# Kernel optimization log

Measured on AMD Instinct MI355X. Metric: run time of the kernel, lower is better.

## Reference

```python
import jax, jax.numpy as jnp
import numpy as np

N = 100_000   # nodes
E = 1_600_000 # edges
G = 128       # graphs in batch
DIN, DOUT = 100, 200


def setup_inputs() -> dict:
    key = jax.random.key(0)
    ks = jax.random.split(key, 12)
    def lin_w(k, fan_in, fan_out):
        return (jax.random.normal(k, (fan_in, fan_out), jnp.float32) / np.sqrt(fan_in)).astype(jnp.float32)
    return {
        "x": jax.random.normal(ks[0], (N, DIN), jnp.float32),
        "edge_index": jax.random.randint(ks[1], (2, E), 0, N, dtype=jnp.int32),
        "batch": jnp.sort(jax.random.randint(ks[2], (N,), 0, G, dtype=jnp.int32)),
        "W1": lin_w(ks[3], DIN, DOUT),  "b1": jnp.zeros((DOUT,), jnp.float32),
        "Wc": lin_w(ks[4], DOUT, DOUT), "bc": jnp.zeros((DOUT,), jnp.float32),
        "W2": lin_w(ks[5], DOUT, DOUT), "b2": jnp.zeros((DOUT,), jnp.float32),
        "W3": lin_w(ks[6], DOUT, DOUT), "b3": jnp.zeros((DOUT,), jnp.float32),
        "Wcls": lin_w(ks[7], DOUT, 2),  "bcls": jnp.zeros((2,), jnp.float32),
    }


def gcn_conv(x, W, b, src, dst, n_nodes):
    """PyG GCNConv: D^{-1/2}(A+I)D^{-1/2} X W + b, symmetric norm with self-loops."""
    h = x @ W  # [N, Dout]
    # degree at targets including the self-loop (+1)
    deg = jax.ops.segment_sum(jnp.ones((src.shape[0],), x.dtype), dst, num_segments=n_nodes) + 1.0
    dinv = jax.lax.rsqrt(deg)  # [N]
    # gather -> normalize -> scatter-add (messages along edges)
    msg = h[src] * (dinv[src] * dinv[dst])[:, None]          # [E, Dout]
    agg = jax.ops.segment_sum(msg, dst, num_segments=n_nodes)  # [N, Dout]
    # self-loop contribution handled analytically: norm_ii = dinv[i]^2
    agg = agg + h * (dinv * dinv)[:, None]
    return agg + b


def reference(x, edge_index, batch, W1, b1, Wc, bc, W2, b2, W3, b3, Wcls, bcls):
    src, dst = edge_index[0], edge_index[1]
    h = jax.nn.relu(gcn_conv(x, W1, b1, src, dst, N))
    # dropout is identity at eval time
    h = h @ Wc + bc
    h = jax.nn.relu(gcn_conv(h, W2, b2, src, dst, N))
    h = gcn_conv(h, W3, b3, src, dst, N)
    pooled = jax.ops.segment_max(h, batch, num_segments=G)  # global max pool -> [G, Dout]
    logits = pooled @ Wcls + bcls
    return jax.nn.softmax(logits, axis=1)
```

## Files before the change

kernel.cpp:

```cpp
#include <hip/hip_runtime.h>
#include <stdint.h>

#define N_NODES 100000
#define N_EDGES 1600000
#define N_GRAPHS 128
#define DIN 100
#define DOUT 200
#define LDH 200
#define LDX 128

#define NB 391
#define BCAP 5120
#define EPB 2048
#define NBLK 782

typedef unsigned short u16;
typedef unsigned int u32;
typedef _Float16 f16;
typedef f16 half8 __attribute__((ext_vector_type(8)));
typedef f16 half4 __attribute__((ext_vector_type(4)));
typedef f16 half2v __attribute__((ext_vector_type(2)));
typedef float floatx4 __attribute__((ext_vector_type(4)));

__device__ __forceinline__ float h2f(u16 h) {
  f16 x; __builtin_memcpy(&x, &h, 2); return (float)x;
}
__device__ __forceinline__ u16 f2h(float f) {
  f16 x = (f16)f; u16 r; __builtin_memcpy(&r, &x, 2); return r;
}

__device__ __forceinline__ void pack_frag(const float* __restrict__ W, int K, int nfrag,
                                          u16* __restrict__ out, int idx) {
  if (idx >= nfrag) return;
  int lane = idx & 63;
  int t = idx >> 6;
  int ct = t % 13, ks = t / 13;
  int n = ct * 16 + (lane & 15);
  int kbase = ks * 32 + (lane >> 4) * 8;
  u16 v[8];
  #pragma unroll
  for (int j = 0; j < 8; ++j) {
    int k = kbase + j;
    float f = (k < K && n < DOUT) ? W[(size_t)k * DOUT + n] : 0.f;
    v[j] = f2h(f);
  }
  uint4 o;
  o.x = (u32)v[0] | ((u32)v[1] << 16);
  o.y = (u32)v[2] | ((u32)v[3] << 16);
  o.z = (u32)v[4] | ((u32)v[5] << 16);
  o.w = (u32)v[6] | ((u32)v[7] << 16);
  *(uint4*)(out + (size_t)idx * 8) = o;
}

#define B_GB    391
#define B_COMB  549
#define B_PK1   562
#define B_PK3   585
#define B_TOT   (585 + NBLK)
__global__ void k_prep(const int* __restrict__ batch, int* __restrict__ gstart,
                       int* __restrict__ gend, const int* __restrict__ dst,
                       int* __restrict__ histAll,
                       const float* __restrict__ Wc, const float* __restrict__ bc,
                       const float* __restrict__ W2, float* __restrict__ Wc2,
                       float* __restrict__ bc2, const float* __restrict__ W1,
                       const float* __restrict__ W3, u16* __restrict__ Wpk1,
                       u16* __restrict__ Wpk3) {
  int b = blockIdx.x, t = threadIdx.x;
  if (b < B_GB) {
    int i = b * 256 + t;
    if (i >= N_NODES) return;
    int g = batch[i];
    if (i == 0 || batch[i - 1] != g) gstart[g] = i;
    if (i == N_NODES - 1 || batch[i + 1] != g) gend[g] = i;
  } else if (b < B_COMB) {
    int gid = (b - B_GB) * 256 + t;
    if (gid >= 201 * DOUT) return;
    int r = gid / DOUT, c = gid % DOUT;
    const float* a = (r < DOUT) ? (Wc + (size_t)r * DOUT) : bc;
    float s = 0.f;
    for (int k = 0; k < DOUT; ++k) s += a[k] * W2[(size_t)k * DOUT + c];
    if (r < DOUT) Wc2[(size_t)r * DOUT + c] = s;
    else bc2[c] = s;
  } else if (b < B_PK1) {
    pack_frag(W1, DIN, 4 * 13 * 64, Wpk1, (b - B_COMB) * 256 + t);
  } else if (b < B_PK3) {
    pack_frag(W3, DOUT, 7 * 13 * 64, Wpk3, (b - B_PK1) * 256 + t);
  } else {
    __shared__ int hist[NB];
    int hb = b - B_PK3;
    int e0 = hb * EPB;
    int e1 = min(e0 + EPB, N_EDGES);
    for (int j = t; j < NB; j += 256) hist[j] = 0;
    __syncthreads();
    for (int i = e0 + t; i < e1; i += 256)
      atomicAdd(&hist[dst[i] >> 8], 1);
    __syncthreads();
    for (int j = t; j < NB; j += 256)
      histAll[(size_t)hb * NB + j] = hist[j];
  }
}

__global__ void k_scan(const int* __restrict__ histAll, int* __restrict__ baseAll,
                       int* __restrict__ gcur) {
  __shared__ int s[256];
  int j = blockIdx.x, t = threadIdx.x;
  int run = 0;
  for (int c = 0; c < NBLK; c += 256) {
    int idx = c + t;
    int v = (idx < NBLK) ? histAll[(size_t)idx * NB + j] : 0;
    s[t] = v;
    __syncthreads();
    for (int o = 1; o < 256; o <<= 1) {
      int x = (t >= o) ? s[t - o] : 0;
      __syncthreads();
      s[t] += x;
      __syncthreads();
    }
    if (idx < NBLK) baseAll[(size_t)idx * NB + j] = run + s[t] - v;
    run += s[255];
    __syncthreads();
  }
  if (t == 0) gcur[j] = run;
}

__global__ void k_scatter(const int* __restrict__ src, const int* __restrict__ dst,
                          const int* __restrict__ baseAll, uint2* __restrict__ ebuf) {
  __shared__ int cur[NB];
  int b = blockIdx.x, t = threadIdx.x;
  int e0 = b * EPB;
  int e1 = min(e0 + EPB, N_EDGES);
  for (int j = t; j < NB; j += 256) cur[j] = baseAll[(size_t)b * NB + j];
  __syncthreads();
  for (int i = e0 + t; i < e1; i += 256) {
    int d = dst[i];
    int bk = d >> 8;
    int pos = atomicAdd(&cur[bk], 1);
    if (pos < BCAP)
      ebuf[(size_t)bk * BCAP + pos] = make_uint2((u32)d, (u32)src[i]);
  }
}

__global__ void k_csr(const uint2* __restrict__ ebuf, const int* __restrict__ gcur,
                      int* __restrict__ rowptr, float* __restrict__ dinv,
                      int* __restrict__ colv) {
  __shared__ int s_cnt[256];
  __shared__ int s_cur[256];
  __shared__ int s_scan[256];
  __shared__ int s_g[NB];
  __shared__ int s_red[256];
  int b = blockIdx.x, t = threadIdx.x;
  for (int j = t; j < NB; j += 256) s_g[j] = gcur[j];
  s_cnt[t] = 0;
  __syncthreads();
  int pacc = 0;
  for (int i = t; i < b; i += 256) pacc += s_g[i];
  s_red[t] = pacc;
  __syncthreads();
  for (int o = 128; o > 0; o >>= 1) {
    if (t < o) s_red[t] += s_red[t + o];
    __syncthreads();
  }
  int base = s_red[0];
  if (b == NB - 1 && t == 0) rowptr[N_NODES] = base + s_g[b];
  int cnt = s_g[b];
  int node0 = b << 8;
  const uint2* eb = ebuf + (size_t)b * BCAP;
  for (int i = t; i < cnt; i += 256)
    atomicAdd(&s_cnt[eb[i].x & 255], 1);
  __syncthreads();
  int v = s_cnt[t];
  s_scan[t] = v;
  __syncthreads();
  for (int o = 1; o < 256; o <<= 1) {
    int x = (t >= o) ? s_scan[t - o] : 0;
    __syncthreads();
    s_scan[t] += x;
    __syncthreads();
  }
  int run = s_scan[t] - v;
  s_cur[t] = base + run;
  int node = node0 + t;
  if (node < N_NODES) {
    rowptr[node] = base + run;
    dinv[node] = rsqrtf((float)v + 1.0f);
  }
  __syncthreads();
  for (int i = t; i < cnt; i += 256) {
    uint2 e = eb[i];
    int pos = atomicAdd(&s_cur[e.x & 255], 1);
    colv[pos] = (int)e.y;
  }
}

#define P_XS  25000
#define P_TOT 25023
__global__ void k_post(const float* __restrict__ x, const float* __restrict__ dinv,
                       u16* __restrict__ xs, const float* __restrict__ Wc2,
                       u16* __restrict__ Wpk2) {
  int b = blockIdx.x, t = threadIdx.x;
  if (b < P_XS) {
    int gid = b * 256 + t;
    int node = gid >> 6, lane = gid & 63;
    if (node >= N_NODES || lane >= 50) return;
    float d = dinv[node];
    float2 vv = *(const float2*)(x + (size_t)node * DIN + lane * 2);
    half2v o; o[0] = (f16)(d * vv.x); o[1] = (f16)(d * vv.y);
    *(half2v*)(xs + (size_t)node * LDX + lane * 2) = o;
  } else {
    pack_frag(Wc2, DOUT, 7 * 13 * 64, Wpk2, (b - P_XS) * 256 + t);
  }
}

template <int NKS>
__global__ __launch_bounds__(256) void k_gemm_mfma(const u16* __restrict__ A, int lda,
                                                   const u16* __restrict__ Wpk,
                                                   const float* __restrict__ bias,
                                                   const float* __restrict__ rowscale,
                                                   u16* __restrict__ C, int relu, int nrows) {
  int wv = threadIdx.x >> 6;
  int lane = threadIdx.x & 63;
  int r0 = blockIdx.x * 128 + wv * 32;
  int m = lane & 15, q = lane >> 4;
  int row0 = r0 + m, row1 = r0 + 16 + m;
  bool ok0 = (row0 < nrows), ok1 = (row1 < nrows);
  const u16* a0p = A + (size_t)row0 * lda + q * 8;
  const u16* a1p = A + (size_t)row1 * lda + q * 8;

  floatx4 acc0[13], acc1[13];
  #pragma unroll
  for (int ct = 0; ct < 13; ++ct) {
    acc0[ct] = floatx4{0.f, 0.f, 0.f, 0.f};
    acc1[ct] = floatx4{0.f, 0.f, 0.f, 0.f};
  }

  const u16* wp = Wpk + (size_t)lane * 8;
  #pragma unroll
  for (int ks = 0; ks < NKS; ++ks) {
    half8 a0 = ok0 ? *(const half8*)(a0p + ks * 32) : half8{0, 0, 0, 0, 0, 0, 0, 0};
    half8 a1 = ok1 ? *(const half8*)(a1p + ks * 32) : half8{0, 0, 0, 0, 0, 0, 0, 0};
    #pragma unroll
    for (int ct = 0; ct < 13; ++ct) {
      half8 bfr = *(const half8*)(wp + (size_t)(ks * 13 + ct) * 512);
      acc0[ct] = __builtin_amdgcn_mfma_f32_16x16x32_f16(a0, bfr, acc0[ct], 0, 0, 0);
      acc1[ct] = __builtin_amdgcn_mfma_f32_16x16x32_f16(a1, bfr, acc1[ct], 0, 0, 0);
    }
  }

  float sc0[4], sc1[4];
  #pragma unroll
  for (int rg = 0; rg < 4; ++rg) {
    int or0 = r0 + q * 4 + rg;
    int or1 = r0 + 16 + q * 4 + rg;
    sc0[rg] = (rowscale && or0 < nrows) ? rowscale[or0] : 1.f;
    sc1[rg] = (rowscale && or1 < nrows) ? rowscale[or1] : 1.f;
  }

  #pragma unroll
  for (int ct = 0; ct < 13; ++ct) {
    int c = ct * 16 + m;
    if (c >= DOUT) continue;
    float bv = bias ? bias[c] : 0.f;
    #pragma unroll
    for (int rg = 0; rg < 4; ++rg) {
      int or0 = r0 + q * 4 + rg;
      if (or0 < nrows) {
        float v = acc0[ct][rg] + bv;
        if (relu) v = fmaxf(v, 0.f);
        C[(size_t)or0 * LDH + c] = f2h(v * sc0[rg]);
      }
      int or1 = r0 + 16 + q * 4 + rg;
      if (or1 < nrows) {
        float v = acc1[ct][rg] + bv;
        if (relu) v = fmaxf(v, 0.f);
        C[(size_t)or1 * LDH + c] = f2h(v * sc1[rg]);
      }
    }
  }
}

__global__ void k_agg200h(const u16* __restrict__ T, const float* __restrict__ dinv,
                          const int* __restrict__ rowptr, const int* __restrict__ col,
                          const float* __restrict__ bias, u16* __restrict__ OUT,
                          int relu) {
  int wave = (blockIdx.x * blockDim.x + threadIdx.x) >> 6;
  int lane = threadIdx.x & 63;
  int n0 = wave * 4;
  if (n0 >= N_NODES) return;
  int rpl = rowptr[n0 + (lane < 4 ? lane : 4)];
  if (lane >= 50) return;
  int c4 = lane * 4;
  for (int i = 0; i < 4; ++i) {
    int node = n0 + i;
    int beg = __builtin_amdgcn_readlane(rpl, i);
    int end = __builtin_amdgcn_readlane(rpl, i + 1);
    half4 sv = *(const half4*)(T + (size_t)node * LDH + c4);
    float di = dinv[node];
    float ax = 0.f, ay = 0.f, az = 0.f, aw = 0.f;
    int e = beg;
    for (; e + 16 <= end; e += 16) {
      int s[16];
      half4 tv[16];
      #pragma unroll
      for (int j = 0; j < 16; ++j) s[j] = col[e + j];
      #pragma unroll
      for (int j = 0; j < 16; ++j)
        tv[j] = *(const half4*)(T + (size_t)s[j] * LDH + c4);
      #pragma unroll
      for (int j = 0; j < 16; ++j) {
        ax += (float)tv[j][0]; ay += (float)tv[j][1];
        az += (float)tv[j][2]; aw += (float)tv[j][3];
      }
    }
    if (e + 8 <= end) {
      int s[8];
      half4 tv[8];
      #pragma unroll
      for (int j = 0; j < 8; ++j) s[j] = col[e + j];
      #pragma unroll
      for (int j = 0; j < 8; ++j)
        tv[j] = *(const half4*)(T + (size_t)s[j] * LDH + c4);
      #pragma unroll
      for (int j = 0; j < 8; ++j) {
        ax += (float)tv[j][0]; ay += (float)tv[j][1];
        az += (float)tv[j][2]; aw += (float)tv[j][3];
      }
      e += 8;
    }
    if (e + 4 <= end) {
      int s[4];
      half4 tv[4];
      #pragma unroll
      for (int j = 0; j < 4; ++j) s[j] = col[e + j];
      #pragma unroll
      for (int j = 0; j < 4; ++j)
        tv[j] = *(const half4*)(T + (size_t)s[j] * LDH + c4);
      #pragma unroll
      for (int j = 0; j < 4; ++j) {
        ax += (float)tv[j][0]; ay += (float)tv[j][1];
        az += (float)tv[j][2]; aw += (float)tv[j][3];
      }
      e += 4;
    }
    for (; e < end; ++e) {
      half4 tv = *(const half4*)(T + (size_t)col[e] * LDH + c4);
      ax += (float)tv[0]; ay += (float)tv[1];
      az += (float)tv[2]; aw += (float)tv[3];
    }
    float rx = di * (ax + (float)sv[0]);
    float ry = di * (ay + (float)sv[1]);
    float rz = di * (az + (float)sv[2]);
    float rw = di * (aw + (float)sv[3]);
    if (bias) {
      rx += bias[c4 + 0]; ry += bias[c4 + 1];
      rz += bias[c4 + 2]; rw += bias[c4 + 3];
    }
    if (relu) {
      rx = fmaxf(rx, 0.f); ry = fmaxf(ry, 0.f);
      rz = fmaxf(rz, 0.f); rw = fmaxf(rw, 0.f);
    }
    half4 o;
    o[0] = (f16)rx; o[1] = (f16)ry; o[2] = (f16)rz; o[3] = (f16)rw;
    __builtin_nontemporal_store(o, (half4*)(OUT + (size_t)node * LDH + c4));
  }
}

__global__ void k_agg100h(const u16* __restrict__ T, const float* __restrict__ dinv,
                          const int* __restrict__ rowptr, const int* __restrict__ col,
                          u16* __restrict__ OUT) {
  int wave = (blockIdx.x * blockDim.x + threadIdx.x) >> 6;
  int lane = threadIdx.x & 63;
  int n0 = wave * 4;
  if (n0 >= N_NODES) return;
  int rpl = rowptr[n0 + (lane < 4 ? lane : 4)];
  if (lane >= 50) return;
  int c2 = lane * 2;
  for (int i = 0; i < 4; ++i) {
    int node = n0 + i;
    int beg = __builtin_amdgcn_readlane(rpl, i);
    int end = __builtin_amdgcn_readlane(rpl, i + 1);
    half2v sv = *(const half2v*)(T + (size_t)node * LDX + c2);
    float di = dinv[node];
    float ax = 0.f, ay = 0.f;
    int e = beg;
    for (; e + 16 <= end; e += 16) {
      int s[16];
      half2v tv[16];
      #pragma unroll
      for (int j = 0; j < 16; ++j) s[j] = col[e + j];
      #pragma unroll
      for (int j = 0; j < 16; ++j)
        tv[j] = *(const half2v*)(T + (size_t)s[j] * LDX + c2);
      #pragma unroll
      for (int j = 0; j < 16; ++j) { ax += (float)tv[j][0]; ay += (float)tv[j][1]; }
    }
    if (e + 8 <= end) {
      int s[8];
      half2v tv[8];
      #pragma unroll
      for (int j = 0; j < 8; ++j) s[j] = col[e + j];
      #pragma unroll
      for (int j = 0; j < 8; ++j)
        tv[j] = *(const half2v*)(T + (size_t)s[j] * LDX + c2);
      #pragma unroll
      for (int j = 0; j < 8; ++j) { ax += (float)tv[j][0]; ay += (float)tv[j][1]; }
      e += 8;
    }
    if (e + 4 <= end) {
      int s[4];
      half2v tv[4];
      #pragma unroll
      for (int j = 0; j < 4; ++j) s[j] = col[e + j];
      #pragma unroll
      for (int j = 0; j < 4; ++j)
        tv[j] = *(const half2v*)(T + (size_t)s[j] * LDX + c2);
      #pragma unroll
      for (int j = 0; j < 4; ++j) { ax += (float)tv[j][0]; ay += (float)tv[j][1]; }
      e += 4;
    }
    for (; e < end; ++e) {
      half2v tv = *(const half2v*)(T + (size_t)col[e] * LDX + c2);
      ax += (float)tv[0]; ay += (float)tv[1];
    }
    half2v o;
    o[0] = (f16)(di * (ax + (float)sv[0]));
    o[1] = (f16)(di * (ay + (float)sv[1]));
    __builtin_nontemporal_store(o, (half2v*)(OUT + (size_t)node * LDX + c2));
  }
}

#define POOL_CHUNKS 8
__global__ void k_pool1h(const u16* __restrict__ H, const int* __restrict__ gstart,
                         const int* __restrict__ gend, float* __restrict__ part) {
  int g = blockIdx.x, c = blockIdx.y, t = threadIdx.x;
  if (t >= 100) return;
  int s = gstart[g], e = gend[g];
  float m0 = -3.4e38f, m1 = -3.4e38f;
  if (s >= 0 && e >= s && e < N_NODES) {
    int len = e - s + 1;
    int cs = s + (int)(((long long)len * c) / POOL_CHUNKS);
    int ce = s + (int)(((long long)len * (c + 1)) / POOL_CHUNKS);
    for (int i = cs; i < ce; ++i) {
      half2v v = *(const half2v*)(H + (size_t)i * LDH + t * 2);
      m0 = fmaxf(m0, (float)v[0]);
      m1 = fmaxf(m1, (float)v[1]);
    }
  }
  float* p = part + (size_t)(g * POOL_CHUNKS + c) * DOUT;
  p[t * 2 + 0] = m0;
  p[t * 2 + 1] = m1;
}

__global__ void k_poolcls(const float* __restrict__ part, const float* __restrict__ Wcls,
                          const float* __restrict__ bcls, float* __restrict__ out) {
  __shared__ float l0s[256], l1s[256];
  int g = blockIdx.x, t = threadIdx.x;
  float c0 = 0.f, c1 = 0.f;
  if (t < DOUT) {
    float m = -3.4e38f;
    #pragma unroll
    for (int c = 0; c < POOL_CHUNKS; ++c)
      m = fmaxf(m, part[(size_t)(g * POOL_CHUNKS + c) * DOUT + t]);
    c0 = m * Wcls[t * 2 + 0];
    c1 = m * Wcls[t * 2 + 1];
  }
  l0s[t] = c0; l1s[t] = c1;
  __syncthreads();
  for (int o = 128; o > 0; o >>= 1) {
    if (t < o) { l0s[t] += l0s[t + o]; l1s[t] += l1s[t + o]; }
    __syncthreads();
  }
  if (t == 0) {
    float l0 = l0s[0] + bcls[0], l1 = l1s[0] + bcls[1];
    float m = fmaxf(l0, l1);
    float e0 = expf(l0 - m), e1 = expf(l1 - m);
    float inv = 1.0f / (e0 + e1);
    out[g * 2 + 0] = e0 * inv;
    out[g * 2 + 1] = e1 * inv;
  }
}

static inline size_t align256(size_t x) { return (x + 255) & ~(size_t)255; }

extern "C" void kernel_launch(void* const* d_in, const int* in_sizes, int n_in,
                              void* d_out, int out_size, void* d_ws, size_t ws_size,
                              hipStream_t stream) {
  const float* x     = (const float*)d_in[0];
  const int*   ei    = (const int*)d_in[1];
  const int*   batch = (const int*)d_in[2];
  const float* W1    = (const float*)d_in[3];
  const float* b1    = (const float*)d_in[4];
  const float* Wc    = (const float*)d_in[5];
  const float* bc    = (const float*)d_in[6];
  const float* W2    = (const float*)d_in[7];
  const float* b2    = (const float*)d_in[8];
  const float* W3    = (const float*)d_in[9];
  const float* b3    = (const float*)d_in[10];
  const float* Wcls  = (const float*)d_in[11];
  const float* bcls  = (const float*)d_in[12];
  float* out = (float*)d_out;

  const int N = N_NODES, E = N_EDGES;
  const int* src = ei;
  const int* dst = ei + E;

  char* ws = (char*)d_ws;
  size_t off = 0;
  float* dinv    = (float*)(ws + off); off = align256(off + (size_t)N * 4);
  int*   rowptr  = (int*)  (ws + off); off = align256(off + (size_t)(N + 1) * 4);
  int*   col     = (int*)  (ws + off); off = align256(off + (size_t)E * 4);
  int*   gcur    = (int*)  (ws + off); off = align256(off + (size_t)NB * 4);
  int*   histAll = (int*)  (ws + off); off = align256(off + (size_t)NBLK * NB * 4);
  int*   baseAll = (int*)  (ws + off); off = align256(off + (size_t)NBLK * NB * 4);
  int*   gstart  = (int*)  (ws + off); off = align256(off + 512);
  int*   gend    = (int*)  (ws + off); off = align256(off + 512);
  float* Wc2     = (float*)(ws + off); off = align256(off + (size_t)DOUT * DOUT * 4);
  float* bc2     = (float*)(ws + off); off = align256(off + (size_t)DOUT * 4);
  u16*   Wpk1    = (u16*)  (ws + off); off = align256(off + (size_t)4 * 13 * 64 * 8 * 2);
  u16*   Wpk2    = (u16*)  (ws + off); off = align256(off + (size_t)7 * 13 * 64 * 8 * 2);
  u16*   Wpk3    = (u16*)  (ws + off); off = align256(off + (size_t)7 * 13 * 64 * 8 * 2);
  u16*   xs      = (u16*)  (ws + off); off = align256(off + ((size_t)N * LDX + 128) * 2);
  u16*   bufX    = (u16*)  (ws + off); off = align256(off + ((size_t)N * LDX + 128) * 2);
  u16*   buf0    = (u16*)  (ws + off); off = align256(off + ((size_t)N * LDH + 128) * 2);
  u16*   buf1    = (u16*)  (ws + off); off = align256(off + ((size_t)N * LDH + 128) * 2);
  u16*   buf2    = (u16*)  (ws + off); off = align256(off + ((size_t)N * LDH + 128) * 2);

  uint2* ebuf = (uint2*)buf0;
  float* part = (float*)buf1;

  k_prep<<<B_TOT, 256, 0, stream>>>(batch, gstart, gend, dst, histAll,
                                    Wc, bc, W2, Wc2, bc2, W1, W3, Wpk1, Wpk3);
  k_scan<<<NB, 256, 0, stream>>>(histAll, baseAll, gcur);
  k_scatter<<<NBLK, 256, 0, stream>>>(src, dst, baseAll, ebuf);
  k_csr<<<NB, 256, 0, stream>>>(ebuf, gcur, rowptr, dinv, col);
  k_post<<<P_TOT, 256, 0, stream>>>(x, dinv, xs, Wc2, Wpk2);

  int gemmb = (N + 127) / 128;
  int aggb  = (N + 15) / 16;

  k_agg100h<<<aggb, 256, 0, stream>>>(xs, dinv, rowptr, col, bufX);
  k_gemm_mfma<4><<<gemmb, 256, 0, stream>>>(bufX, LDX, Wpk1, b1, nullptr, buf0, 1, N);
  k_gemm_mfma<7><<<gemmb, 256, 0, stream>>>(buf0, LDH, Wpk2, bc2, dinv, buf2, 0, N);
  k_agg200h<<<aggb, 256, 0, stream>>>(buf2, dinv, rowptr, col, b2, buf0, 1);
  k_gemm_mfma<7><<<gemmb, 256, 0, stream>>>(buf0, LDH, Wpk3, nullptr, dinv, buf1, 0, N);
  k_agg200h<<<aggb, 256, 0, stream>>>(buf1, dinv, rowptr, col, b3, buf2, 0);

  dim3 pg(N_GRAPHS, POOL_CHUNKS);
  k_pool1h<<<pg, 256, 0, stream>>>(buf2, gstart, gend, part);
  k_poolcls<<<N_GRAPHS, 256, 0, stream>>>(part, Wcls, bcls, out);
}
```

Measured before the change: 684.4 us.

## Fuse GEMM pair, fold pooling into last aggregation, merge prep kernels

Runs the first two dense GEMMs in one kernel, keeping the intermediate tile in shared memory. The final aggregation now does the global max pool directly through order-preserving integer atomicMax, which removes the separate pool kernel and one full write of node features. The xs scaling moves into the CSR kernel, W2 packing moves into the scan kernel, and the aggregation kernels switch to one node per wave. The cost is extra launches of smaller waves, atomic contention on pooled outputs, and a memset.

```diff
diff --git a/kernel.cpp b/kernel.cpp
--- a/kernel.cpp
+++ b/kernel.cpp
@@ -8,6 +8,7 @@
 #define DOUT 200
 #define LDH 200
 #define LDX 128
+#define LDT 248
 
 #define NB 391
 #define BCAP 5120
@@ -27,6 +28,10 @@
 }
 __device__ __forceinline__ u16 f2h(float f) {
   f16 x = (f16)f; u16 r; __builtin_memcpy(&r, &x, 2); return r;
+}
+__device__ __forceinline__ u32 encmax(float f) {
+  u32 b; __builtin_memcpy(&b, &f, 4);
+  return (b & 0x80000000u) ? ~b : (b | 0x80000000u);
 }
 
 __device__ __forceinline__ void pack_frag(const float* __restrict__ W, int K, int nfrag,
@@ -100,10 +105,16 @@
   }
 }
 
+#define SCAN_TOT (NB + 23)
 __global__ void k_scan(const int* __restrict__ histAll, int* __restrict__ baseAll,
-                       int* __restrict__ gcur) {
+                       int* __restrict__ gcur, const float* __restrict__ Wc2,
+                       u16* __restrict__ Wpk2) {
+  int j = blockIdx.x, t = threadIdx.x;
+  if (j >= NB) {
+    pack_frag(Wc2, DOUT, 7 * 13 * 64, Wpk2, (j - NB) * 256 + t);
+    return;
+  }
   __shared__ int s[256];
-  int j = blockIdx.x, t = threadIdx.x;
   int run = 0;
   for (int c = 0; c < NBLK; c += 256) {
     int idx = c + t;
@@ -142,12 +153,14 @@
 
 __global__ void k_csr(const uint2* __restrict__ ebuf, const int* __restrict__ gcur,
                       int* __restrict__ rowptr, float* __restrict__ dinv,
-                      int* __restrict__ colv) {
+                      int* __restrict__ colv, const float* __restrict__ x,
+                      u16* __restrict__ xs) {
   __shared__ int s_cnt[256];
   __shared__ int s_cur[256];
   __shared__ int s_scan[256];
   __shared__ int s_g[NB];
   __shared__ int s_red[256];
+  __shared__ float s_dinv[256];
   int b = blockIdx.x, t = threadIdx.x;
   for (int j = t; j < NB; j += 256) s_g[j] = gcur[j];
   s_cnt[t] = 0;
@@ -172,17 +185,19 @@
   s_scan[t] = v;
   __syncthreads();
   for (int o = 1; o < 256; o <<= 1) {
-    int x = (t >= o) ? s_scan[t - o] : 0;
+    int x2 = (t >= o) ? s_scan[t - o] : 0;
     __syncthreads();
-    s_scan[t] += x;
+    s_scan[t] += x2;
     __syncthreads();
   }
   int run = s_scan[t] - v;
   s_cur[t] = base + run;
+  float dval = rsqrtf((float)v + 1.0f);
+  s_dinv[t] = dval;
   int node = node0 + t;
   if (node < N_NODES) {
     rowptr[node] = base + run;
-    dinv[node] = rsqrtf((float)v + 1.0f);
+    dinv[node] = dval;
   }
   __syncthreads();
   for (int i = t; i < cnt; i += 256) {
@@ -190,24 +205,117 @@
     int pos = atomicAdd(&s_cur[e.x & 255], 1);
     colv[pos] = (int)e.y;
   }
-}
-
-#define P_XS  25000
-#define P_TOT 25023
-__global__ void k_post(const float* __restrict__ x, const float* __restrict__ dinv,
-                       u16* __restrict__ xs, const float* __restrict__ Wc2,
-                       u16* __restrict__ Wpk2) {
-  int b = blockIdx.x, t = threadIdx.x;
-  if (b < P_XS) {
-    int gid = b * 256 + t;
-    int node = gid >> 6, lane = gid & 63;
-    if (node >= N_NODES || lane >= 50) return;
-    float d = dinv[node];
-    float2 vv = *(const float2*)(x + (size_t)node * DIN + lane * 2);
-    half2v o; o[0] = (f16)(d * vv.x); o[1] = (f16)(d * vv.y);
-    *(half2v*)(xs + (size_t)node * LDX + lane * 2) = o;
-  } else {
-    pack_frag(Wc2, DOUT, 7 * 13 * 64, Wpk2, (b - P_XS) * 256 + t);
+  for (int idx = t; idx < 256 * 50; idx += 256) {
+    int nl = idx / 50, c = idx % 50;
+    int nd = node0 + nl;
+    if (nd < N_NODES) {
+      float d = s_dinv[nl];
+      float2 vv = *(const float2*)(x + (size_t)nd * DIN + c * 2);
+      half2v o; o[0] = (f16)(d * vv.x); o[1] = (f16)(d * vv.y);
+      *(half2v*)(xs + (size_t)nd * LDX + c * 2) = o;
+    }
+  }
+}
+
+__global__ __launch_bounds__(256) void k_gemm12(const u16* __restrict__ A,
+                                                const u16* __restrict__ Wpk1,
+                                                const float* __restrict__ b1,
+                                                const u16* __restrict__ Wpk2,
+                                                const float* __restrict__ bc2,
+                                                const float* __restrict__ dinv,
+                                                u16* __restrict__ C, int nrows) {
+  __shared__ u16 tile[4][32][LDT];
+  int wv = threadIdx.x >> 6;
+  int lane = threadIdx.x & 63;
+  int r0 = blockIdx.x * 128 + wv * 32;
+  int m = lane & 15, q = lane >> 4;
+  int row0 = r0 + m, row1 = r0 + 16 + m;
+  bool ok0 = (row0 < nrows), ok1 = (row1 < nrows);
+
+  floatx4 acc0[13], acc1[13];
+  #pragma unroll
+  for (int ct = 0; ct < 13; ++ct) {
+    acc0[ct] = floatx4{0.f, 0.f, 0.f, 0.f};
+    acc1[ct] = floatx4{0.f, 0.f, 0.f, 0.f};
+  }
+
+  {
+    const u16* a0p = A + (size_t)row0 * LDX + q * 8;
+    const u16* a1p = A + (size_t)row1 * LDX + q * 8;
+    const u16* wp = Wpk1 + (size_t)lane * 8;
+    #pragma unroll
+    for (int ks = 0; ks < 4; ++ks) {
+      half8 a0 = ok0 ? *(const half8*)(a0p + ks * 32) : half8{0, 0, 0, 0, 0, 0, 0, 0};
+      half8 a1 = ok1 ? *(const half8*)(a1p + ks * 32) : half8{0, 0, 0, 0, 0, 0, 0, 0};
+      #pragma unroll
+      for (int ct = 0; ct < 13; ++ct) {
+        half8 bfr = *(const half8*)(wp + (size_t)(ks * 13 + ct) * 512);
+        acc0[ct] = __builtin_amdgcn_mfma_f32_16x16x32_f16(a0, bfr, acc0[ct], 0, 0, 0);
+        acc1[ct] = __builtin_amdgcn_mfma_f32_16x16x32_f16(a1, bfr, acc1[ct], 0, 0, 0);
+      }
+    }
+  }
+
+  for (int idx = lane; idx < 32 * ((LDT - 200) / 2); idx += 64) {
+    int rr = idx / ((LDT - 200) / 2);
+    int cc = 200 + (idx % ((LDT - 200) / 2)) * 2;
+    *(half2v*)&tile[wv][rr][cc] = half2v{0, 0};
+  }
+  #pragma unroll
+  for (int ct = 0; ct < 13; ++ct) {
+    int c = ct * 16 + m;
+    if (c >= DOUT) continue;
+    float bv = b1[c];
+    #pragma unroll
+    for (int rg = 0; rg < 4; ++rg) {
+      tile[wv][q * 4 + rg][c]      = f2h(fmaxf(acc0[ct][rg] + bv, 0.f));
+      tile[wv][16 + q * 4 + rg][c] = f2h(fmaxf(acc1[ct][rg] + bv, 0.f));
+    }
+  }
+  __syncthreads();
+
+  #pragma unroll
+  for (int ct = 0; ct < 13; ++ct) {
+    acc0[ct] = floatx4{0.f, 0.f, 0.f, 0.f};
+    acc1[ct] = floatx4{0.f, 0.f, 0.f, 0.f};
+  }
+  {
+    const u16* wp = Wpk2 + (size_t)lane * 8;
+    #pragma unroll
+    for (int ks = 0; ks < 7; ++ks) {
+      half8 a0 = *(const half8*)&tile[wv][m][q * 8 + ks * 32];
+      half8 a1 = *(const half8*)&tile[wv][16 + m][q * 8 + ks * 32];
+      #pragma unroll
+      for (int ct = 0; ct < 13; ++ct) {
+        half8 bfr = *(const half8*)(wp + (size_t)(ks * 13 + ct) * 512);
+        acc0[ct] = __builtin_amdgcn_mfma_f32_16x16x32_f16(a0, bfr, acc0[ct], 0, 0, 0);
+        acc1[ct] = __builtin_amdgcn_mfma_f32_16x16x32_f16(a1, bfr, acc1[ct], 0, 0, 0);
+      }
+    }
+  }
+
+  float sc0[4], sc1[4];
+  #pragma unroll
+  for (int rg = 0; rg < 4; ++rg) {
+    int or0 = r0 + q * 4 + rg;
+    int or1 = r0 + 16 + q * 4 + rg;
+    sc0[rg] = (or0 < nrows) ? dinv[or0] : 1.f;
+    sc1[rg] = (or1 < nrows) ? dinv[or1] : 1.f;
+  }
+  #pragma unroll
+  for (int ct = 0; ct < 13; ++ct) {
+    int c = ct * 16 + m;
+    if (c >= DOUT) continue;
+    float bv = bc2[c];
+    #pragma unroll
+    for (int rg = 0; rg < 4; ++rg) {
+      int or0 = r0 + q * 4 + rg;
+      if (or0 < nrows)
+        C[(size_t)or0 * LDH + c] = f2h((acc0[ct][rg] + bv) * sc0[rg]);
+      int or1 = r0 + 16 + q * 4 + rg;
+      if (or1 < nrows)
+        C[(size_t)or1 * LDH + c] = f2h((acc1[ct][rg] + bv) * sc1[rg]);
+    }
   }
 }
 
@@ -284,84 +392,79 @@
                           int relu) {
   int wave = (blockIdx.x * blockDim.x + threadIdx.x) >> 6;
   int lane = threadIdx.x & 63;
-  int n0 = wave * 4;
-  if (n0 >= N_NODES) return;
-  int rpl = rowptr[n0 + (lane < 4 ? lane : 4)];
-  if (lane >= 50) return;
+  if (wave >= N_NODES || lane >= 50) return;
+  int node = wave;
   int c4 = lane * 4;
-  for (int i = 0; i < 4; ++i) {
-    int node = n0 + i;
-    int beg = __builtin_amdgcn_readlane(rpl, i);
-    int end = __builtin_amdgcn_readlane(rpl, i + 1);
-    half4 sv = *(const half4*)(T + (size_t)node * LDH + c4);
-    float di = dinv[node];
-    float ax = 0.f, ay = 0.f, az = 0.f, aw = 0.f;
-    int e = beg;
-    for (; e + 16 <= end; e += 16) {
-      int s[16];
-      half4 tv[16];
-      #pragma unroll
-      for (int j = 0; j < 16; ++j) s[j] = col[e + j];
-      #pragma unroll
-      for (int j = 0; j < 16; ++j)
-        tv[j] = *(const half4*)(T + (size_t)s[j] * LDH + c4);
-      #pragma unroll
-      for (int j = 0; j < 16; ++j) {
-        ax += (float)tv[j][0]; ay += (float)tv[j][1];
-        az += (float)tv[j][2]; aw += (float)tv[j][3];
-      }
-    }
-    if (e + 8 <= end) {
-      int s[8];
-      half4 tv[8];
-      #pragma unroll
-      for (int j = 0; j < 8; ++j) s[j] = col[e + j];
-      #pragma unroll
-      for (int j = 0; j < 8; ++j)
-        tv[j] = *(const half4*)(T + (size_t)s[j] * LDH + c4);
-      #pragma unroll
-      for (int j = 0; j < 8; ++j) {
-        ax += (float)tv[j][0]; ay += (float)tv[j][1];
-        az += (float)tv[j][2]; aw += (float)tv[j][3];
-      }
-      e += 8;
-    }
-    if (e + 4 <= end) {
-      int s[4];
-      half4 tv[4];
-      #pragma unroll
-      for (int j = 0; j < 4; ++j) s[j] = col[e + j];
-      #pragma unroll
-      for (int j = 0; j < 4; ++j)
-        tv[j] = *(const half4*)(T + (size_t)s[j] * LDH + c4);
-      #pragma unroll
-      for (int j = 0; j < 4; ++j) {
-        ax += (float)tv[j][0]; ay += (float)tv[j][1];
-        az += (float)tv[j][2]; aw += (float)tv[j][3];
-      }
-      e += 4;
-    }
-    for (; e < end; ++e) {
-      half4 tv = *(const half4*)(T + (size_t)col[e] * LDH + c4);
-      ax += (float)tv[0]; ay += (float)tv[1];
-      az += (float)tv[2]; aw += (float)tv[3];
-    }
-    float rx = di * (ax + (float)sv[0]);
-    float ry = di * (ay + (float)sv[1]);
-    float rz = di * (az + (float)sv[2]);
-    float rw = di * (aw + (float)sv[3]);
-    if (bias) {
-      rx += bias[c4 + 0]; ry += bias[c4 + 1];
-      rz += bias[c4 + 2]; rw += bias[c4 + 3];
-    }
-    if (relu) {
-      rx = fmaxf(rx, 0.f); ry = fmaxf(ry, 0.f);
-      rz = fmaxf(rz, 0.f); rw = fmaxf(rw, 0.f);
-    }
-    half4 o;
-    o[0] = (f16)rx; o[1] = (f16)ry; o[2] = (f16)rz; o[3] = (f16)rw;
-    __builtin_nontemporal_store(o, (half4*)(OUT + (size_t)node * LDH + c4));
-  }
+  int beg = __builtin_amdgcn_readfirstlane(rowptr[node]);
+  int end = __builtin_amdgcn_readfirstlane(rowptr[node + 1]);
+  half4 sv = *(const half4*)(T + (size_t)node * LDH + c4);
+  float di = dinv[node];
+  float ax = 0.f, ay = 0.f, az = 0.f, aw = 0.f;
+  int e = beg;
+  for (; e + 16 <= end; e += 16) {
+    int s[16];
+    half4 tv[16];
+    #pragma unroll
+    for (int j = 0; j < 16; ++j) s[j] = col[e + j];
+    #pragma unroll
+    for (int j = 0; j < 16; ++j)
+      tv[j] = *(const half4*)(T + (size_t)s[j] * LDH + c4);
+    #pragma unroll
+    for (int j = 0; j < 16; ++j) {
+      ax += (float)tv[j][0]; ay += (float)tv[j][1];
+      az += (float)tv[j][2]; aw += (float)tv[j][3];
+    }
+  }
+  if (e + 8 <= end) {
+    int s[8];
+    half4 tv[8];
+    #pragma unroll
+    for (int j = 0; j < 8; ++j) s[j] = col[e + j];
+    #pragma unroll
+    for (int j = 0; j < 8; ++j)
+      tv[j] = *(const half4*)(T + (size_t)s[j] * LDH + c4);
+    #pragma unroll
+    for (int j = 0; j < 8; ++j) {
+      ax += (float)tv[j][0]; ay += (float)tv[j][1];
+      az += (float)tv[j][2]; aw += (float)tv[j][3];
+    }
+    e += 8;
+  }
+  if (e + 4 <= end) {
+    int s[4];
+    half4 tv[4];
+    #pragma unroll
+    for (int j = 0; j < 4; ++j) s[j] = col[e + j];
+    #pragma unroll
+    for (int j = 0; j < 4; ++j)
+      tv[j] = *(const half4*)(T + (size_t)s[j] * LDH + c4);
+    #pragma unroll
+    for (int j = 0; j < 4; ++j) {
+      ax += (float)tv[j][0]; ay += (float)tv[j][1];
+      az += (float)tv[j][2]; aw += (float)tv[j][3];
+    }
+    e += 4;
+  }
+  for (; e < end; ++e) {
+    half4 tv = *(const half4*)(T + (size_t)col[e] * LDH + c4);
+    ax += (float)tv[0]; ay += (float)tv[1];
+    az += (float)tv[2]; aw += (float)tv[3];
+  }
+  float rx = di * (ax + (float)sv[0]);
+  float ry = di * (ay + (float)sv[1]);
+  float rz = di * (az + (float)sv[2]);
+  float rw = di * (aw + (float)sv[3]);
+  if (bias) {
+    rx += bias[c4 + 0]; ry += bias[c4 + 1];
+    rz += bias[c4 + 2]; rw += bias[c4 + 3];
+  }
+  if (relu) {
+    rx = fmaxf(rx, 0.f); ry = fmaxf(ry, 0.f);
+    rz = fmaxf(rz, 0.f); rw = fmaxf(rw, 0.f);
+  }
+  half4 o;
+  o[0] = (f16)rx; o[1] = (f16)ry; o[2] = (f16)rz; o[3] = (f16)rw;
+  __builtin_nontemporal_store(o, (half4*)(OUT + (size_t)node * LDH + c4));
 }
 
 __global__ void k_agg100h(const u16* __restrict__ T, const float* __restrict__ dinv,
@@ -369,99 +472,177 @@
                           u16* __restrict__ OUT) {
   int wave = (blockIdx.x * blockDim.x + threadIdx.x) >> 6;
   int lane = threadIdx.x & 63;
-  int n0 = wave * 4;
-  if (n0 >= N_NODES) return;
+  if (wave >= N_NODES || lane >= 50) return;
+  int node = wave;
+  int c2 = lane * 2;
+  int beg = __builtin_amdgcn_readfirstlane(rowptr[node]);
+  int end = __builtin_amdgcn_readfirstlane(rowptr[node + 1]);
+  half2v sv = *(const half2v*)(T + (size_t)node * LDX + c2);
+  float di = dinv[node];
+  float ax = 0.f, ay = 0.f;
+  int e = beg;
+  for (; e + 16 <= end; e += 16) {
+    int s[16];
+    half2v tv[16];
+    #pragma unroll
+    for (int j = 0; j < 16; ++j) s[j] = col[e + j];
+    #pragma unroll
+    for (int j = 0; j < 16; ++j)
+      tv[j] = *(const half2v*)(T + (size_t)s[j] * LDX + c2);
+    #pragma unroll
+    for (int j = 0; j < 16; ++j) { ax += (float)tv[j][0]; ay += (float)tv[j][1]; }
+  }
+  if (e + 8 <= end) {
+    int s[8];
+    half2v tv[8];
+    #pragma unroll
+    for (int j = 0; j < 8; ++j) s[j] = col[e + j];
+    #pragma unroll
+    for (int j = 0; j < 8; ++j)
+      tv[j] = *(const half2v*)(T + (size_t)s[j] * LDX + c2);
+    #pragma unroll
+    for (int j = 0; j < 8; ++j) { ax += (float)tv[j][0]; ay += (float)tv[j][1]; }
+    e += 8;
+  }
+  if (e + 4 <= end) {
+    int s[4];
+    half2v tv[4];
+    #pragma unroll
+    for (int j = 0; j < 4; ++j) s[j] = col[e + j];
+    #pragma unroll
+    for (int j = 0; j < 4; ++j)
+      tv[j] = *(const half2v*)(T + (size_t)s[j] * LDX + c2);
+    #pragma unroll
+    for (int j = 0; j < 4; ++j) { ax += (float)tv[j][0]; ay += (float)tv[j][1]; }
+    e += 4;
+  }
+  for (; e < end; ++e) {
+    half2v tv = *(const half2v*)(T + (size_t)col[e] * LDX + c2);
+    ax += (float)tv[0]; ay += (float)tv[1];
+  }
+  half2v o;
+  o[0] = (f16)(di * (ax + (float)sv[0]));
+  o[1] = (f16)(di * (ay + (float)sv[1]));
+  __builtin_nontemporal_store(o, (half2v*)(OUT + (size_t)node * LDX + c2));
+}
+
+__global__ void k_aggpool(const u16* __restrict__ T, const float* __restrict__ dinv,
+                          const int* __restrict__ rowptr, const int* __restrict__ col,
+                          const float* __restrict__ bias, const int* __restrict__ batch,
+                          u32* __restrict__ partenc) {
+  __shared__ u32 s_enc[4][DOUT];
+  int t = threadIdx.x;
+  for (int i = t; i < 4 * DOUT; i += 256) ((u32*)s_enc)[i] = 0u;
+  __syncthreads();
+  int wv = t >> 6, lane = t & 63;
+  int nb0 = blockIdx.x * 16;
+  int n0 = nb0 + wv * 4;
+  int gfirst = batch[nb0];
   int rpl = rowptr[n0 + (lane < 4 ? lane : 4)];
-  if (lane >= 50) return;
-  int c2 = lane * 2;
-  for (int i = 0; i < 4; ++i) {
-    int node = n0 + i;
-    int beg = __builtin_amdgcn_readlane(rpl, i);
-    int end = __builtin_amdgcn_readlane(rpl, i + 1);
-    half2v sv = *(const half2v*)(T + (size_t)node * LDX + c2);
-    float di = dinv[node];
-    float ax = 0.f, ay = 0.f;
-    int e = beg;
-    for (; e + 16 <= end; e += 16) {
-      int s[16];
-      half2v tv[16];
-      #pragma unroll
-      for (int j = 0; j < 16; ++j) s[j] = col[e + j];
-      #pragma unroll
-      for (int j = 0; j < 16; ++j)
-        tv[j] = *(const half2v*)(T + (size_t)s[j] * LDX + c2);
-      #pragma unroll
-      for (int j = 0; j < 16; ++j) { ax += (float)tv[j][0]; ay += (float)tv[j][1]; }
-    }
-    if (e + 8 <= end) {
-      int s[8];
-      half2v tv[8];
-      #pragma unroll
-      for (int j = 0; j < 8; ++j) s[j] = col[e + j];
-      #pragma unroll
-      for (int j = 0; j < 8; ++j)
-        tv[j] = *(const half2v*)(T + (size_t)s[j] * LDX + c2);
-      #pragma unroll
-      for (int j = 0; j < 8; ++j) { ax += (float)tv[j][0]; ay += (float)tv[j][1]; }
-      e += 8;
-    }
-    if (e + 4 <= end) {
-      int s[4];
-      half2v tv[4];
-      #pragma unroll
-      for (int j = 0; j < 4; ++j) s[j] = col[e + j];
-      #pragma unroll
-      for (int j = 0; j < 4; ++j)
-        tv[j] = *(const half2v*)(T + (size_t)s[j] * LDX + c2);
-      #pragma unroll
-      for (int j = 0; j < 4; ++j) { ax += (float)tv[j][0]; ay += (float)tv[j][1]; }
-      e += 4;
-    }
-    for (; e < end; ++e) {
-      half2v tv = *(const half2v*)(T + (size_t)col[e] * LDX + c2);
-      ax += (float)tv[0]; ay += (float)tv[1];
-    }
-    half2v o;
-    o[0] = (f16)(di * (ax + (float)sv[0]));
-    o[1] = (f16)(di * (ay + (float)sv[1]));
-    __builtin_nontemporal_store(o, (half2v*)(OUT + (size_t)node * LDX + c2));
-  }
-}
-
-#define POOL_CHUNKS 8
-__global__ void k_pool1h(const u16* __restrict__ H, const int* __restrict__ gstart,
-                         const int* __restrict__ gend, float* __restrict__ part) {
-  int g = blockIdx.x, c = blockIdx.y, t = threadIdx.x;
-  if (t >= 100) return;
-  int s = gstart[g], e = gend[g];
-  float m0 = -3.4e38f, m1 = -3.4e38f;
-  if (s >= 0 && e >= s && e < N_NODES) {
-    int len = e - s + 1;
-    int cs = s + (int)(((long long)len * c) / POOL_CHUNKS);
-    int ce = s + (int)(((long long)len * (c + 1)) / POOL_CHUNKS);
-    for (int i = cs; i < ce; ++i) {
-      half2v v = *(const half2v*)(H + (size_t)i * LDH + t * 2);
-      m0 = fmaxf(m0, (float)v[0]);
-      m1 = fmaxf(m1, (float)v[1]);
-    }
-  }
-  float* p = part + (size_t)(g * POOL_CHUNKS + c) * DOUT;
-  p[t * 2 + 0] = m0;
-  p[t * 2 + 1] = m1;
-}
-
-__global__ void k_poolcls(const float* __restrict__ part, const float* __restrict__ Wcls,
+  if (lane < 50) {
+    int c4 = lane * 4;
+    float b0 = bias[c4 + 0], b1v = bias[c4 + 1], b2v = bias[c4 + 2], b3v = bias[c4 + 3];
+    for (int i = 0; i < 4; ++i) {
+      int node = n0 + i;
+      int beg = __builtin_amdgcn_readlane(rpl, i);
+      int end = __builtin_amdgcn_readlane(rpl, i + 1);
+      half4 sv = *(const half4*)(T + (size_t)node * LDH + c4);
+      float di = dinv[node];
+      float ax = 0.f, ay = 0.f, az = 0.f, aw = 0.f;
+      int e = beg;
+      for (; e + 16 <= end; e += 16) {
+        int s[16];
+        half4 tv[16];
+        #pragma unroll
+        for (int j = 0; j < 16; ++j) s[j] = col[e + j];
+        #pragma unroll
+        for (int j = 0; j < 16; ++j)
+          tv[j] = *(const half4*)(T + (size_t)s[j] * LDH + c4);
+        #pragma unroll
+        for (int j = 0; j < 16; ++j) {
+          ax += (float)tv[j][0]; ay += (float)tv[j][1];
+          az += (float)tv[j][2]; aw += (float)tv[j][3];
+        }
+      }
+      if (e + 8 <= end) {
+        int s[8];
+        half4 tv[8];
+        #pragma unroll
+        for (int j = 0; j < 8; ++j) s[j] = col[e + j];
+        #pragma unroll
+        for (int j = 0; j < 8; ++j)
+          tv[j] = *(const half4*)(T + (size_t)s[j] * LDH + c4);
+        #pragma unroll
+        for (int j = 0; j < 8; ++j) {
+          ax += (float)tv[j][0]; ay += (float)tv[j][1];
+          az += (float)tv[j][2]; aw += (float)tv[j][3];
+        }
+        e += 8;
+      }
+      if (e + 4 <= end) {
+        int s[4];
+        half4 tv[4];
+        #pragma unroll
+        for (int j = 0; j < 4; ++j) s[j] = col[e + j];
+        #pragma unroll
+        for (int j = 0; j < 4; ++j)
+          tv[j] = *(const half4*)(T + (size_t)s[j] * LDH + c4);
+        #pragma unroll
+        for (int j = 0; j < 4; ++j) {
+          ax += (float)tv[j][0]; ay += (float)tv[j][1];
+          az += (float)tv[j][2]; aw += (float)tv[j][3];
+        }
+        e += 4;
+      }
+      for (; e < end; ++e) {
+        half4 tv = *(const half4*)(T + (size_t)col[e] * LDH + c4);
+        ax += (float)tv[0]; ay += (float)tv[1];
+        az += (float)tv[2]; aw += (float)tv[3];
+      }
+      float rx = di * (ax + (float)sv[0]) + b0;
+      float ry = di * (ay + (float)sv[1]) + b1v;
+      float rz = di * (az + (float)sv[2]) + b2v;
+      float rw = di * (aw + (float)sv[3]) + b3v;
+      u32 e0 = encmax(rx), e1 = encmax(ry), e2 = encmax(rz), e3 = encmax(rw);
+      int slot = batch[node] - gfirst;
+      if (slot < 4) {
+        atomicMax(&s_enc[slot][c4 + 0], e0);
+        atomicMax(&s_enc[slot][c4 + 1], e1);
+        atomicMax(&s_enc[slot][c4 + 2], e2);
+        atomicMax(&s_enc[slot][c4 + 3], e3);
+      } else {
+        u32* p = partenc + (size_t)batch[node] * DOUT + c4;
+        atomicMax(&p[0], e0); atomicMax(&p[1], e1);
+        atomicMax(&p[2], e2); atomicMax(&p[3], e3);
+      }
+    }
+  }
+  __syncthreads();
+  for (int i = t; i < 4 * DOUT; i += 256) {
+    u32 v = ((u32*)s_enc)[i];
+    if (v) {
+      int slot = i / DOUT, d = i % DOUT;
+      atomicMax(&partenc[(size_t)(gfirst + slot) * DOUT + d], v);
+    }
+  }
+}
+
+__global__ void k_poolcls(const u32* __restrict__ partenc, const float* __restrict__ Wcls,
                           const float* __restrict__ bcls, float* __restrict__ out) {
   __shared__ float l0s[256], l1s[256];
   int g = blockIdx.x, t = threadIdx.x;
   float c0 = 0.f, c1 = 0.f;
   if (t < DOUT) {
-    float m = -3.4e38f;
-    #pragma unroll
-    for (int c = 0; c < POOL_CHUNKS; ++c)
-      m = fmaxf(m, part[(size_t)(g * POOL_CHUNKS + c) * DOUT + t]);
-    c0 = m * Wcls[t * 2 + 0];
-    c1 = m * Wcls[t * 2 + 1];
+    u32 e = partenc[(size_t)g * DOUT + t];
+    float mv;
+    if (e == 0u) {
+      mv = -3.4e38f;
+    } else {
+      u32 b = (e & 0x80000000u) ? (e ^ 0x80000000u) : ~e;
+      __builtin_memcpy(&mv, &b, 4);
+    }
+    c0 = mv * Wcls[t * 2 + 0];
+    c1 = mv * Wcls[t * 2 + 1];
   }
   l0s[t] = c0; l1s[t] = c1;
   __syncthreads();
@@ -524,27 +705,24 @@
   u16*   buf1    = (u16*)  (ws + off); off = align256(off + ((size_t)N * LDH + 128) * 2);
   u16*   buf2    = (u16*)  (ws + off); off = align256(off + ((size_t)N * LDH + 128) * 2);
 
-  uint2* ebuf = (uint2*)buf0;
-  float* part = (float*)buf1;
+  uint2* ebuf    = (uint2*)buf0;
+  u32*   partenc = (u32*)bufX;
 
   k_prep<<<B_TOT, 256, 0, stream>>>(batch, gstart, gend, dst, histAll,
                                     Wc, bc, W2, Wc2, bc2, W1, W3, Wpk1, Wpk3);
-  k_scan<<<NB, 256, 0, stream>>>(histAll, baseAll, gcur);
+  k_scan<<<SCAN_TOT, 256, 0, stream>>>(histAll, baseAll, gcur, Wc2, Wpk2);
   k_scatter<<<NBLK, 256, 0, stream>>>(src, dst, baseAll, ebuf);
-  k_csr<<<NB, 256, 0, stream>>>(ebuf, gcur, rowptr, dinv, col);
-  k_post<<<P_TOT, 256, 0, stream>>>(x, dinv, xs, Wc2, Wpk2);
+  k_csr<<<NB, 256, 0, stream>>>(ebuf, gcur, rowptr, dinv, col, x, xs);
 
   int gemmb = (N + 127) / 128;
-  int aggb  = (N + 15) / 16;
+  int aggb  = (N + 3) / 4;
+  int aggpb = N / 16;
 
   k_agg100h<<<aggb, 256, 0, stream>>>(xs, dinv, rowptr, col, bufX);
-  k_gemm_mfma<4><<<gemmb, 256, 0, stream>>>(bufX, LDX, Wpk1, b1, nullptr, buf0, 1, N);
-  k_gemm_mfma<7><<<gemmb, 256, 0, stream>>>(buf0, LDH, Wpk2, bc2, dinv, buf2, 0, N);
+  k_gemm12<<<gemmb, 256, 0, stream>>>(bufX, Wpk1, b1, Wpk2, bc2, dinv, buf2, N);
+  hipMemsetAsync(partenc, 0, (size_t)N_GRAPHS * DOUT * 4, stream);
   k_agg200h<<<aggb, 256, 0, stream>>>(buf2, dinv, rowptr, col, b2, buf0, 1);
   k_gemm_mfma<7><<<gemmb, 256, 0, stream>>>(buf0, LDH, Wpk3, nullptr, dinv, buf1, 0, N);
-  k_agg200h<<<aggb, 256, 0, stream>>>(buf1, dinv, rowptr, col, b3, buf2, 0);
-
-  dim3 pg(N_GRAPHS, POOL_CHUNKS);
-  k_pool1h<<<pg, 256, 0, stream>>>(buf2, gstart, gend, part);
-  k_poolcls<<<N_GRAPHS, 256, 0, stream>>>(part, Wcls, bcls, out);
-}
+  k_aggpool<<<aggpb, 256, 0, stream>>>(buf1, dinv, rowptr, col, b3, batch, partenc);
+  k_poolcls<<<N_GRAPHS, 256, 0, stream>>>(partenc, Wcls, bcls, out);
+}
```

Measured after the change: 653.4 us. -4.5%, faster.
